# Kernel optimization log

Measured on AMD Instinct MI355X. Metric: run time of the kernel, lower is better.

The kernel has to match this reference:

```python
import jax, jax.numpy as jnp
import numpy as np

N_EXPERTS = 8
TOP_K = 2
AUX_COEF = 0.01
Z_COEF = 0.001


def setup_inputs() -> dict:
    key = jax.random.key(0)
    ks = jax.random.split(key, 5)
    B, S, D, F, E = 2, 2048, 768, 2048, N_EXPERTS
    std = 0.02
    std_out = std / np.sqrt(2 * 12)  # scale_init_by_depth, n_layers=12
    return {
        "x": jax.random.normal(ks[0], (B, S, D), jnp.float32),
        "router_w": jax.random.normal(ks[1], (D, E), jnp.float32) * std,
        "w1": jax.random.normal(ks[2], (E, D, F), jnp.float32) * std,
        "w2": jax.random.normal(ks[3], (E, F, D), jnp.float32) * std_out,
        "w3": jax.random.normal(ks[4], (E, D, F), jnp.float32) * std,
    }


def reference(x, router_w, w1, w2, w3):
    B, S, D = x.shape
    E = w1.shape[0]
    x_flat = x.reshape(-1, D)                      # [N, D]
    n_tokens = x_flat.shape[0]

    router_logits = x_flat @ router_w               # [N, E]
    probs = jax.nn.softmax(router_logits.astype(jnp.float32), axis=-1)
    topk_w, topk_i = jax.lax.top_k(probs, TOP_K)    # [N, K]
    topk_w = topk_w / jnp.sum(topk_w, axis=-1, keepdims=True)

    # Combine: equivalent to sort/group dispatch + per-expert GEMM + index_add,
    # expressed as a masked per-expert (fixed, small E) dense pass.
    out = jnp.zeros((n_tokens, D), dtype=x.dtype)
    for e in range(E):
        gate = jnp.sum(jnp.where(topk_i == e, topk_w, 0.0), axis=-1)  # [N] f32
        h = jax.nn.silu(x_flat @ w1[e]) * (x_flat @ w3[e])            # [N, F]
        out = out + gate[:, None].astype(x.dtype) * (h @ w2[e])

    # Switch-style load-balancing aux loss + z-loss
    importance = probs.mean(axis=0)                 # [E]
    top1 = topk_i[:, 0]
    load = jnp.zeros((E,), jnp.float32).at[top1].add(1.0) / n_tokens
    aux_loss = E * jnp.sum(importance * load) * AUX_COEF
    z_loss = jnp.mean(router_logits.astype(jnp.float32) ** 2) * Z_COEF

    return out.reshape(B, S, D), aux_loss, z_loss
```

## Files before the change

### kernel.cpp

```cpp
#include <hip/hip_runtime.h>
#include <hip/hip_bf16.h>

constexpr int NT = 4096;
constexpr int DD = 768;
constexpr int FF = 2048;
constexpr int NE = 8;
constexpr int MAXROWS = 9216;
constexpr int MAXMT128 = 72;
constexpr int MAXMT256 = 40;
constexpr int NKT1 = DD / 64;
constexpr int NKT2 = FF / 64;

constexpr int IDX_CNTA   = 0;
constexpr int IDX_CNTT1  = 8;
constexpr int IDX_CUR    = 16;
constexpr int IDX_IMP    = 24;
constexpr int IDX_ZSUM   = 32;
constexpr int IDX_NTILES = 33;
constexpr int IDX_OFF    = 34;
constexpr int IDX_EXPT   = 48;
constexpr int IDX_N256   = 120;
constexpr int IDX_E256   = 128;
constexpr int IDX_B256   = 168;
constexpr int IDX_L256   = 208;

constexpr size_t OFF_META   = 0;
constexpr size_t OFF_TKE    = 1024;
constexpr size_t OFF_GATE   = OFF_TKE    + (size_t)NT*2*4;
constexpr size_t OFF_ROWOF  = OFF_GATE   + (size_t)NT*2*4;
constexpr size_t OFF_TOKROW = OFF_ROWOF  + (size_t)NT*2*4;
constexpr size_t OFF_XG     = 136192;
constexpr size_t OFF_W1T    = OFF_XG  + (size_t)MAXROWS*DD*2;
constexpr size_t OFF_W3T    = OFF_W1T + (size_t)NE*FF*DD*2;
constexpr size_t OFF_W2T    = OFF_W3T + (size_t)NE*FF*DD*2;
constexpr size_t OFF_H      = OFF_W2T + (size_t)NE*FF*DD*2;
constexpr size_t OFF_OP     = OFF_H   + (size_t)MAXROWS*FF*2;

typedef float f32x4 __attribute__((ext_vector_type(4)));
typedef __bf16 bf16x8v __attribute__((ext_vector_type(8)));
typedef unsigned short u16x8 __attribute__((ext_vector_type(8)));

__device__ inline unsigned short f2bf_bits(float f) {
  __bf16 h = (__bf16)f;
  return *(unsigned short*)&h;
}
__device__ inline float bf2f(unsigned short u) {
  unsigned v = (unsigned)u << 16;
  return *(float*)&v;
}

__device__ __forceinline__ void glds16(const void* g, void* l) {
  __builtin_amdgcn_global_load_lds(
      (const __attribute__((address_space(1))) unsigned int*)g,
      (__attribute__((address_space(3))) unsigned int*)l, 16, 0, 0);
}

constexpr int RB = 128;
__global__ __launch_bounds__(256) void router_kernel(const float* __restrict__ x,
    const float* __restrict__ rw, int* __restrict__ meta,
    int* __restrict__ tke, float* __restrict__ gateArr) {
  __shared__ float s_imp[NE];
  __shared__ float s_z;
  __shared__ int s_cnt1[NE], s_cnta[NE];
  if (threadIdx.x < NE) { s_imp[threadIdx.x] = 0.f; s_cnt1[threadIdx.x] = 0; s_cnta[threadIdx.x] = 0; }
  if (threadIdx.x == 0) s_z = 0.f;
  __syncthreads();

  const int wave = threadIdx.x >> 6, lane = threadIdx.x & 63;
  float impacc[NE];
  #pragma unroll
  for (int e = 0; e < NE; ++e) impacc[e] = 0.f;
  float zacc = 0.f;

  for (int t = blockIdx.x * 4 + wave; t < NT; t += RB * 4) {
    float acc[NE];
    #pragma unroll
    for (int e = 0; e < NE; ++e) acc[e] = 0.f;
    const float* xr = x + (size_t)t * DD;
    for (int i = lane; i < DD; i += 64) {
      float xv = xr[i];
      const float* r = rw + i * NE;
      #pragma unroll
      for (int e = 0; e < NE; ++e) acc[e] += xv * r[e];
    }
    #pragma unroll
    for (int off = 32; off > 0; off >>= 1) {
      #pragma unroll
      for (int e = 0; e < NE; ++e) acc[e] += __shfl_xor(acc[e], off);
    }
    float mx = acc[0];
    #pragma unroll
    for (int e = 1; e < NE; ++e) mx = fmaxf(mx, acc[e]);
    float p[NE]; float s = 0.f;
    #pragma unroll
    for (int e = 0; e < NE; ++e) { p[e] = __expf(acc[e] - mx); s += p[e]; }
    float inv = 1.f / s;
    #pragma unroll
    for (int e = 0; e < NE; ++e) p[e] *= inv;
    int e0 = 0; float p0 = p[0];
    #pragma unroll
    for (int e = 1; e < NE; ++e) if (p[e] > p0) { p0 = p[e]; e0 = e; }
    int e1 = -1; float p1 = -1.f;
    #pragma unroll
    for (int e = 0; e < NE; ++e) if (e != e0 && p[e] > p1) { p1 = p[e]; e1 = e; }
    if (lane == 0) {
      #pragma unroll
      for (int e = 0; e < NE; ++e) { impacc[e] += p[e]; zacc += acc[e] * acc[e]; }
      atomicAdd(&s_cnt1[e0], 1);
      atomicAdd(&s_cnta[e0], 1);
      atomicAdd(&s_cnta[e1], 1);
      float gs = 1.f / (p0 + p1);
      tke[t*2]   = e0; tke[t*2+1] = e1;
      gateArr[t*2] = p0 * gs; gateArr[t*2+1] = p1 * gs;
    }
  }
  if (lane == 0) {
    #pragma unroll
    for (int e = 0; e < NE; ++e) atomicAdd(&s_imp[e], impacc[e]);
    atomicAdd(&s_z, zacc);
  }
  __syncthreads();
  float* fmeta = (float*)meta;
  if (threadIdx.x < NE) {
    atomicAdd(&fmeta[IDX_IMP + threadIdx.x], s_imp[threadIdx.x]);
    atomicAdd(&meta[IDX_CNTT1 + threadIdx.x], s_cnt1[threadIdx.x]);
    atomicAdd(&meta[IDX_CNTA + threadIdx.x], s_cnta[threadIdx.x]);
  }
  if (threadIdx.x == NE) atomicAdd(&fmeta[IDX_ZSUM], s_z);
}

__global__ __launch_bounds__(128) void scan_kernel(int* __restrict__ meta,
                                                   float* __restrict__ out_tail) {
  __shared__ int s_off[NE + 1];
  __shared__ int s_nt[NE];
  __shared__ float s_aux;
  const int t = threadIdx.x;
  if (t < NE) s_nt[t] = (meta[IDX_CNTA + t] + 127) >> 7;
  __syncthreads();
  if (t == 0) {
    int off = 0;
    for (int e = 0; e < NE; ++e) { s_off[e] = off; off += s_nt[e]; }
    s_off[NE] = off;
  }
  __syncthreads();
  const int ntiles = s_off[NE];
  if (t < NE) meta[IDX_OFF + t] = s_off[t] << 7;
  if (t == NE) { meta[IDX_OFF + NE] = ntiles << 7; meta[IDX_NTILES] = ntiles; }
  if (t < ntiles) {
    int e = 0;
    while (t >= s_off[e + 1]) e++;
    meta[IDX_EXPT + t] = e;
  }
  if (t == 0) {
    int n2t = 0;
    for (int e = 0; e < NE; ++e) {
      const int base = s_off[e] << 7;
      const int lim  = base + (s_nt[e] << 7);
      const int n2 = (s_nt[e] + 1) >> 1;
      for (int i = 0; i < n2; ++i) {
        meta[IDX_E256 + n2t] = e;
        meta[IDX_B256 + n2t] = base + (i << 8);
        meta[IDX_L256 + n2t] = lim;
        ++n2t;
      }
    }
    meta[IDX_N256] = n2t;
  }
  float* fmeta = (float*)meta;
  float pl = 0.f;
  if (t < NE)
    pl = (fmeta[IDX_IMP + t] / (float)NT) * ((float)meta[IDX_CNTT1 + t] / (float)NT);
  if (t < 64) {
    #pragma unroll
    for (int off = 4; off > 0; off >>= 1) pl += __shfl_xor(pl, off);
    if (t == 0) s_aux = pl;
  }
  __syncthreads();
  if (t == 0) {
    out_tail[0] = (float)NE * s_aux * 0.01f;
    out_tail[1] = fmeta[IDX_ZSUM] / (float)(NT * NE) * 0.001f;
  }
}

__global__ __launch_bounds__(256) void scatter_kernel(const int* __restrict__ tke,
    int* __restrict__ meta, int* __restrict__ rowof, int* __restrict__ tokrow) {
  __shared__ int s_cnt[NE], s_base[NE];
  const int t = blockIdx.x * 256 + threadIdx.x;
  if (threadIdx.x < NE) s_cnt[threadIdx.x] = 0;
  __syncthreads();
  const int e0 = tke[t*2], e1 = tke[t*2 + 1];
  const int l0 = atomicAdd(&s_cnt[e0], 1);
  const int l1 = atomicAdd(&s_cnt[e1], 1);
  __syncthreads();
  if (threadIdx.x < NE)
    s_base[threadIdx.x] = atomicAdd(&meta[IDX_CUR + threadIdx.x], s_cnt[threadIdx.x]);
  __syncthreads();
  const int r0 = meta[IDX_OFF + e0] + s_base[e0] + l0;
  const int r1 = meta[IDX_OFF + e1] + s_base[e1] + l1;
  rowof[t*2]     = r0;
  rowof[t*2 + 1] = r1;
  tokrow[r0] = t;
  tokrow[r1] = t;
}

__global__ __launch_bounds__(192) void gather_kernel(const float* __restrict__ x,
    const int* __restrict__ tokrow, const int* __restrict__ meta,
    __bf16* __restrict__ Xg) {
  const int row = blockIdx.x;
  if (row >= meta[IDX_OFF + NE]) return;
  const int tok = tokrow[row];
  ushort4* dst = (ushort4*)(Xg + (size_t)row * DD);
  const int i = threadIdx.x;
  ushort4 o;
  if (tok >= 0) {
    float4 v = ((const float4*)(x + (size_t)tok * DD))[i];
    o.x = f2bf_bits(v.x); o.y = f2bf_bits(v.y);
    o.z = f2bf_bits(v.z); o.w = f2bf_bits(v.w);
  } else {
    o.x = o.y = o.z = o.w = 0;
  }
  dst[i] = o;
}

constexpr int TS = 68;
__global__ __launch_bounds__(256) void transpose_cvt_all(
    const float* __restrict__ w1, const float* __restrict__ w3,
    const float* __restrict__ w2, __bf16* __restrict__ W1t,
    __bf16* __restrict__ W3t, __bf16* __restrict__ W2t) {
  const int z = blockIdx.z, which = z >> 3, e = z & 7;
  const float* src; __bf16* dst; int R, C, rt, ct;
  if (which == 0)      { src = w1; dst = W1t; R = DD; C = FF; rt = blockIdx.y; ct = blockIdx.x; }
  else if (which == 1) { src = w3; dst = W3t; R = DD; C = FF; rt = blockIdx.y; ct = blockIdx.x; }
  else                 { src = w2; dst = W2t; R = FF; C = DD; rt = blockIdx.x; ct = blockIdx.y; }
  src += (size_t)e * DD * FF; dst += (size_t)e * DD * FF;
  const int r0 = rt * 64, c0 = ct * 64;
  __shared__ __align__(16) __bf16 tile[64 * TS];
  const int t = threadIdx.x;
  #pragma unroll
  for (int i = 0; i < 4; ++i) {
    int idx = t + i * 256; int r = idx >> 4, q = idx & 15;
    float4 v = *(const float4*)&src[(size_t)(r0 + r) * C + c0 + q * 4];
    ushort4 o;
    o.x = f2bf_bits(v.x); o.y = f2bf_bits(v.y);
    o.z = f2bf_bits(v.z); o.w = f2bf_bits(v.w);
    *(ushort4*)&tile[r * TS + q * 4] = o;
  }
  __syncthreads();
  #pragma unroll
  for (int i = 0; i < 2; ++i) {
    int idx = t + i * 256; int c = idx >> 3, seg = idx & 7;
    u16x8 o;
    #pragma unroll
    for (int k = 0; k < 8; ++k)
      o[k] = *(unsigned short*)&tile[(seg * 8 + k) * TS + c];
    *(u16x8*)&dst[(size_t)(c0 + c) * R + r0 + seg * 8] = o;
  }
}

__global__ __launch_bounds__(512, 2) void gemm1_kernel(
    const __bf16* __restrict__ Xg, const __bf16* __restrict__ W1t,
    const __bf16* __restrict__ W3t, __bf16* __restrict__ Hb,
    const int* __restrict__ meta) {
  const int mt = blockIdx.y;
  if (mt >= meta[IDX_N256]) return;
  const int e      = meta[IDX_E256 + mt];
  const int m0     = meta[IDX_B256 + mt];
  const int rowlim = meta[IDX_L256 + mt];
  const int n0 = blockIdx.x * 128;

  __shared__ __align__(16) __bf16 As[2][256 * 64];
  __shared__ __align__(16) __bf16 Bs[2][256 * 64];

  const int t = threadIdx.x, lane = t & 63, wid = t >> 6;
  const int wm = wid >> 2, wn = wid & 3;
  const int lane15 = lane & 15, g = lane >> 4;

  const __bf16* __restrict__ W1e = W1t + (size_t)e * FF * DD;
  const __bf16* __restrict__ W3e = W3t + (size_t)e * FF * DD;

  const int aBase = (wm * 128 + lane15) * 64;
  const int bBase = (wn * 64 + lane15) * 64;
  const int c0 = ((g    ) ^ (lane & 7)) * 8;
  const int c1 = ((4 + g) ^ (lane & 7)) * 8;

  const int o0v = t, o1v = 512 + t;
  const int r0v = o0v >> 3, r1v = o1v >> 3;
  const int cl0 = (o0v & 7) ^ (r0v & 7), cl1 = (o1v & 7) ^ (r1v & 7);
  int gA00 = m0 + r0v;        if (gA00 >= MAXROWS) gA00 = 0;
  int gA01 = m0 + r1v;        if (gA01 >= MAXROWS) gA01 = 0;
  int gA10 = m0 + 128 + r0v;  if (gA10 >= MAXROWS) gA10 = 0;
  int gA11 = m0 + 128 + r1v;  if (gA11 >= MAXROWS) gA11 = 0;
  const __bf16* aS00 = Xg + (size_t)gA00 * DD + cl0 * 8;
  const __bf16* aS01 = Xg + (size_t)gA01 * DD + cl1 * 8;
  const __bf16* aS10 = Xg + (size_t)gA10 * DD + cl0 * 8;
  const __bf16* aS11 = Xg + (size_t)gA11 * DD + cl1 * 8;
  const int fc0 = n0 + ((r0v >> 5) << 4) + (r0v & 15);
  const int fc1 = n0 + ((r1v >> 5) << 4) + (r1v & 15);
  const __bf16* bW0 = (r0v & 16) ? W3e : W1e;
  const __bf16* bW1 = (r1v & 16) ? W3e : W1e;
  const __bf16* bS00 = bW0 + (size_t)fc0 * DD + cl0 * 8;
  const __bf16* bS01 = bW1 + (size_t)fc1 * DD + cl1 * 8;
  const __bf16* bS10 = bW0 + (size_t)(fc0 + 64) * DD + cl0 * 8;
  const __bf16* bS11 = bW1 + (size_t)(fc1 + 64) * DD + cl1 * 8;
  const int L00 = (       wid * 64) * 8;
  const int L01 = ( 512 + wid * 64) * 8;
  const int L10 = (1024 + wid * 64) * 8;
  const int L11 = (1536 + wid * 64) * 8;

  auto st2 = [&](__bf16* dstBuf, int kt, const __bf16* s0, const __bf16* s1,
                 int d0, int d1) {
    glds16(s0 + (size_t)kt * 64, dstBuf + d0);
    glds16(s1 + (size_t)kt * 64, dstBuf + d1);
  };

  const f32x4 zero = {0.f, 0.f, 0.f, 0.f};
  f32x4 acc[8][4];
  #pragma unroll
  for (int i = 0; i < 8; ++i)
    #pragma unroll
    for (int j = 0; j < 4; ++j) acc[i][j] = zero;

  __bf16 *Ac = &As[0][0], *An = &As[1][0];
  __bf16 *Bc = &Bs[0][0], *Bn = &Bs[1][0];

  st2(Ac, 0, aS00, aS01, L00, L01); st2(Ac, 0, aS10, aS11, L10, L11);
  st2(Bc, 0, bS00, bS01, L00, L01); st2(Bc, 0, bS10, bS11, L10, L11);
  st2(An, 1, aS00, aS01, L00, L01); st2(An, 1, aS10, aS11, L10, L11);
  st2(Bn, 1, bS00, bS01, L00, L01); st2(Bn, 1, bS10, bS11, L10, L11);
  asm volatile("s_waitcnt vmcnt(8)" ::: "memory");
  __builtin_amdgcn_s_barrier();

  bf16x8v af[8], ag[8], bf[8];

  for (int k = 0; k < NKT1; ++k) {
    const bool k2ok = (k < NKT1 - 2);
    #pragma unroll
    for (int i = 0; i < 4; ++i) {
      af[i*2+0] = *(const bf16x8v*)&Ac[aBase + i*1024 + c0];
      af[i*2+1] = *(const bf16x8v*)&Ac[aBase + i*1024 + c1];
    }
    #pragma unroll
    for (int j = 0; j < 4; ++j) {
      bf[j*2+0] = *(const bf16x8v*)&Bc[bBase + j*1024 + c0];
      bf[j*2+1] = *(const bf16x8v*)&Bc[bBase + j*1024 + c1];
    }
    __builtin_amdgcn_s_barrier();
    asm volatile("s_waitcnt lgkmcnt(0)" ::: "memory");
    __builtin_amdgcn_s_setprio(1);
    #pragma unroll
    for (int i = 0; i < 4; ++i)
      #pragma unroll
      for (int j = 0; j < 2; ++j) {
        acc[i][j] = __builtin_amdgcn_mfma_f32_16x16x32_bf16(af[i*2+0], bf[j*2+0], acc[i][j], 0, 0, 0);
        acc[i][j] = __builtin_amdgcn_mfma_f32_16x16x32_bf16(af[i*2+1], bf[j*2+1], acc[i][j], 0, 0, 0);
      }
    __builtin_amdgcn_s_setprio(0);
    __builtin_amdgcn_s_barrier();

    #pragma unroll
    for (int i = 0; i < 4; ++i) {
      ag[i*2+0] = *(const bf16x8v*)&Ac[aBase + (4+i)*1024 + c0];
      ag[i*2+1] = *(const bf16x8v*)&Ac[aBase + (4+i)*1024 + c1];
    }
    if (k2ok) st2(Bc, k + 2, bS00, bS01, L00, L01);
    __builtin_amdgcn_s_barrier();
    asm volatile("s_waitcnt lgkmcnt(0)" ::: "memory");
    __builtin_amdgcn_s_setprio(1);
    #pragma unroll
    for (int i = 0; i < 4; ++i)
      #pragma unroll
      for (int j = 0; j < 2; ++j) {
        acc[4+i][j] = __builtin_amdgcn_mfma_f32_16x16x32_bf16(ag[i*2+0], bf[j*2+0], acc[4+i][j], 0, 0, 0);
        acc[4+i][j] = __builtin_amdgcn_mfma_f32_16x16x32_bf16(ag[i*2+1], bf[j*2+1], acc[4+i][j], 0, 0, 0);
      }
    __builtin_amdgcn_s_setprio(0);
    __builtin_amdgcn_s_barrier();

    if (k2ok) {
      st2(Ac, k + 2, aS00, aS01, L00, L01);
      st2(Bc, k + 2, bS10, bS11, L10, L11);
    }
    __builtin_amdgcn_s_barrier();
    __builtin_amdgcn_s_setprio(1);
    #pragma unroll
    for (int i = 0; i < 4; ++i)
      #pragma unroll
      for (int j = 0; j < 2; ++j) {
        acc[i][2+j] = __builtin_amdgcn_mfma_f32_16x16x32_bf16(af[i*2+0], bf[(2+j)*2+0], acc[i][2+j], 0, 0, 0);
        acc[i][2+j] = __builtin_amdgcn_mfma_f32_16x16x32_bf16(af[i*2+1], bf[(2+j)*2+1], acc[i][2+j], 0, 0, 0);
      }
    __builtin_amdgcn_s_setprio(0);
    __builtin_amdgcn_s_barrier();

    if (k2ok) st2(Ac, k + 2, aS10, aS11, L10, L11);
    __builtin_amdgcn_s_barrier();
    __builtin_amdgcn_s_setprio(1);
    #pragma unroll
    for (int i = 0; i < 4; ++i)
      #pragma unroll
      for (int j = 0; j < 2; ++j) {
        acc[4+i][2+j] = __builtin_amdgcn_mfma_f32_16x16x32_bf16(ag[i*2+0], bf[(2+j)*2+0], acc[4+i][2+j], 0, 0, 0);
        acc[4+i][2+j] = __builtin_amdgcn_mfma_f32_16x16x32_bf16(ag[i*2+1], bf[(2+j)*2+1], acc[4+i][2+j], 0, 0, 0);
      }
    __builtin_amdgcn_s_setprio(0);
    if (k2ok)               { asm volatile("s_waitcnt vmcnt(8)" ::: "memory"); }
    else if (k == NKT1 - 2) { asm volatile("s_waitcnt vmcnt(0)" ::: "memory"); }
    __builtin_amdgcn_s_barrier();

    __bf16* tp;
    tp = Ac; Ac = An; An = tp;
    tp = Bc; Bc = Bn; Bn = tp;
  }

  #pragma unroll
  for (int i = 0; i < 8; ++i) {
    const int grow = m0 + wm * 128 + i * 16 + (lane >> 4) * 4;
    #pragma unroll
    for (int p = 0; p < 2; ++p) {
      const int col = n0 + (wn * 2 + p) * 16 + lane15;
      const f32x4 v1 = acc[i][2*p], v3 = acc[i][2*p + 1];
      #pragma unroll
      for (int r = 0; r < 4; ++r) {
        if (grow + r < rowlim) {
          float h = v1[r] / (1.f + __expf(-v1[r])) * v3[r];
          Hb[(size_t)(grow + r) * FF + col] = (__bf16)h;
        }
      }
    }
  }
}

__global__ __launch_bounds__(512, 2) void gemm2_kernel(
    const __bf16* __restrict__ Hb, const __bf16* __restrict__ W2t,
    __bf16* __restrict__ OP, const int* __restrict__ meta) {
  const int mt = blockIdx.y;
  if (mt >= meta[IDX_N256]) return;
  const int e      = meta[IDX_E256 + mt];
  const int m0     = meta[IDX_B256 + mt];
  const int rowlim = meta[IDX_L256 + mt];
  const int n0 = blockIdx.x * 128;

  __shared__ __align__(16) __bf16 As[2][256 * 64];
  __shared__ __align__(16) __bf16 Bs[2][128 * 64];

  const int t = threadIdx.x, lane = t & 63, wid = t >> 6;
  const int wm = wid >> 2, wn = wid & 3;
  const int lane15 = lane & 15, g = lane >> 4;

  const __bf16* __restrict__ W2e = W2t + (size_t)e * DD * FF;

  const int aBase = (wm * 128 + lane15) * 64;
  const int bBase = (wn * 32 + lane15) * 64;
  const int c0 = ((g    ) ^ (lane & 7)) * 8;
  const int c1 = ((4 + g) ^ (lane & 7)) * 8;

  const int o0v = t, o1v = 512 + t;
  const int r0v = o0v >> 3, r1v = o1v >> 3;
  const int cl0 = (o0v & 7) ^ (r0v & 7), cl1 = (o1v & 7) ^ (r1v & 7);
  const int L00 = (       wid * 64) * 8;
  const int L01 = ( 512 + wid * 64) * 8;
  const int L10 = (1024 + wid * 64) * 8;
  const int L11 = (1536 + wid * 64) * 8;

  int gA00 = m0 + r0v;        if (gA00 >= MAXROWS) gA00 = 0;
  int gA01 = m0 + r1v;        if (gA01 >= MAXROWS) gA01 = 0;
  int gA10 = m0 + 128 + r0v;  if (gA10 >= MAXROWS) gA10 = 0;
  int gA11 = m0 + 128 + r1v;  if (gA11 >= MAXROWS) gA11 = 0;
  const __bf16* aS00 = Hb + (size_t)gA00 * FF + cl0 * 8;
  const __bf16* aS01 = Hb + (size_t)gA01 * FF + cl1 * 8;
  const __bf16* aS10 = Hb + (size_t)gA10 * FF + cl0 * 8;
  const __bf16* aS11 = Hb + (size_t)gA11 * FF + cl1 * 8;
  const __bf16* bS0  = W2e + (size_t)(n0 + r0v) * FF + cl0 * 8;
  const __bf16* bS1  = W2e + (size_t)(n0 + r1v) * FF + cl1 * 8;

  auto stA = [&](__bf16* d, int kt) {
    glds16(aS00 + (size_t)kt * 64, d + L00);
    glds16(aS01 + (size_t)kt * 64, d + L01);
    glds16(aS10 + (size_t)kt * 64, d + L10);
    glds16(aS11 + (size_t)kt * 64, d + L11);
  };
  auto stB = [&](__bf16* d, int kt) {
    glds16(bS0 + (size_t)kt * 64, d + L00);
    glds16(bS1 + (size_t)kt * 64, d + L01);
  };

  const f32x4 zero = {0.f, 0.f, 0.f, 0.f};
  f32x4 acc[8][2];
  #pragma unroll
  for (int i = 0; i < 8; ++i)
    #pragma unroll
    for (int j = 0; j < 2; ++j) acc[i][j] = zero;

  __bf16 *Ac = &As[0][0], *An = &As[1][0];
  __bf16 *Bc = &Bs[0][0], *Bn = &Bs[1][0];

  stA(Ac, 0); stB(Bc, 0);
  stA(An, 1); stB(Bn, 1);
  asm volatile("s_waitcnt vmcnt(6)" ::: "memory");
  __builtin_amdgcn_s_barrier();

  bf16x8v af[8], ag[8], bfr[4];

  for (int k = 0; k < NKT2; ++k) {
    const bool k2ok = (k < NKT2 - 2);
    #pragma unroll
    for (int i = 0; i < 4; ++i) {
      af[i*2+0] = *(const bf16x8v*)&Ac[aBase + i*1024 + c0];
      af[i*2+1] = *(const bf16x8v*)&Ac[aBase + i*1024 + c1];
    }
    #pragma unroll
    for (int i = 0; i < 4; ++i) {
      ag[i*2+0] = *(const bf16x8v*)&Ac[aBase + (4+i)*1024 + c0];
      ag[i*2+1] = *(const bf16x8v*)&Ac[aBase + (4+i)*1024 + c1];
    }
    #pragma unroll
    for (int j = 0; j < 2; ++j) {
      bfr[j*2+0] = *(const bf16x8v*)&Bc[bBase + j*1024 + c0];
      bfr[j*2+1] = *(const bf16x8v*)&Bc[bBase + j*1024 + c1];
    }
    __builtin_amdgcn_s_barrier();
    asm volatile("s_waitcnt lgkmcnt(0)" ::: "memory");
    __builtin_amdgcn_s_setprio(1);
    #pragma unroll
    for (int i = 0; i < 4; ++i)
      #pragma unroll
      for (int j = 0; j < 2; ++j) {
        acc[i][j] = __builtin_amdgcn_mfma_f32_16x16x32_bf16(af[i*2+0], bfr[j*2+0], acc[i][j], 0, 0, 0);
        acc[i][j] = __builtin_amdgcn_mfma_f32_16x16x32_bf16(af[i*2+1], bfr[j*2+1], acc[i][j], 0, 0, 0);
      }
    __builtin_amdgcn_s_setprio(0);
    __builtin_amdgcn_s_barrier();

    if (k2ok) { stA(Ac, k + 2); stB(Bc, k + 2); }
    __builtin_amdgcn_s_setprio(1);
    #pragma unroll
    for (int i = 0; i < 4; ++i)
      #pragma unroll
      for (int j = 0; j < 2; ++j) {
        acc[4+i][j] = __builtin_amdgcn_mfma_f32_16x16x32_bf16(ag[i*2+0], bfr[j*2+0], acc[4+i][j], 0, 0, 0);
        acc[4+i][j] = __builtin_amdgcn_mfma_f32_16x16x32_bf16(ag[i*2+1], bfr[j*2+1], acc[4+i][j], 0, 0, 0);
      }
    __builtin_amdgcn_s_setprio(0);
    if (k2ok)               { asm volatile("s_waitcnt vmcnt(6)" ::: "memory"); }
    else if (k == NKT2 - 2) { asm volatile("s_waitcnt vmcnt(0)" ::: "memory"); }
    __builtin_amdgcn_s_barrier();

    __bf16* tp;
    tp = Ac; Ac = An; An = tp;
    tp = Bc; Bc = Bn; Bn = tp;
  }

  #pragma unroll
  for (int i = 0; i < 8; ++i) {
    const int rowb = m0 + wm * 128 + i * 16 + (lane >> 4) * 4;
    #pragma unroll
    for (int jj = 0; jj < 2; ++jj) {
      const int col = n0 + wn * 32 + jj * 16 + lane15;
      #pragma unroll
      for (int r = 0; r < 4; ++r)
        if (rowb + r < rowlim)
          OP[(size_t)(rowb + r) * DD + col] = (__bf16)acc[i][jj][r];
    }
  }
}

__global__ __launch_bounds__(192) void combine_kernel(const __bf16* __restrict__ OP,
    const int* __restrict__ rowof, const float* __restrict__ gateArr,
    float* __restrict__ out) {
  const int t = blockIdx.x;
  const int r0 = rowof[t*2], r1 = rowof[t*2 + 1];
  const float g0 = gateArr[t*2], g1 = gateArr[t*2 + 1];
  const ushort4* p0 = (const ushort4*)(OP + (size_t)r0 * DD);
  const ushort4* p1 = (const ushort4*)(OP + (size_t)r1 * DD);
  const int i = threadIdx.x;
  ushort4 a = p0[i], b = p1[i];
  float4 o;
  o.x = g0 * bf2f(a.x) + g1 * bf2f(b.x);
  o.y = g0 * bf2f(a.y) + g1 * bf2f(b.y);
  o.z = g0 * bf2f(a.z) + g1 * bf2f(b.z);
  o.w = g0 * bf2f(a.w) + g1 * bf2f(b.w);
  ((float4*)(out + (size_t)t * DD))[i] = o;
}

extern "C" void kernel_launch(void* const* d_in, const int* in_sizes, int n_in,
                              void* d_out, int out_size, void* d_ws, size_t ws_size,
                              hipStream_t stream) {
  const float* x  = (const float*)d_in[0];
  const float* rw = (const float*)d_in[1];
  const float* w1 = (const float*)d_in[2];
  const float* w2 = (const float*)d_in[3];
  const float* w3 = (const float*)d_in[4];
  float* out = (float*)d_out;

  char* ws = (char*)d_ws;
  int*    meta   = (int*)(ws + OFF_META);
  int*    tke    = (int*)(ws + OFF_TKE);
  float*  gateA  = (float*)(ws + OFF_GATE);
  int*    rowof  = (int*)(ws + OFF_ROWOF);
  int*    tokrow = (int*)(ws + OFF_TOKROW);
  __bf16* Xg     = (__bf16*)(ws + OFF_XG);
  __bf16* W1t    = (__bf16*)(ws + OFF_W1T);
  __bf16* W3t    = (__bf16*)(ws + OFF_W3T);
  __bf16* W2t    = (__bf16*)(ws + OFF_W2T);
  __bf16* Hb     = (__bf16*)(ws + OFF_H);
  __bf16* OP     = (__bf16*)(ws + OFF_OP);

  hipMemsetAsync(ws + OFF_META, 0, 1024, stream);
  hipMemsetAsync(ws + OFF_TOKROW, 0xFF, (size_t)MAXROWS * 4, stream);

  transpose_cvt_all<<<dim3(32, 12, 24), 256, 0, stream>>>(w1, w3, w2, W1t, W3t, W2t);

  router_kernel<<<RB, 256, 0, stream>>>(x, rw, meta, tke, gateA);
  scan_kernel<<<1, 128, 0, stream>>>(meta, out + (size_t)NT * DD);
  scatter_kernel<<<NT/256, 256, 0, stream>>>(tke, meta, rowof, tokrow);
  gather_kernel<<<MAXROWS, 192, 0, stream>>>(x, tokrow, meta, Xg);

  gemm1_kernel<<<dim3(FF/128, MAXMT256), 512, 0, stream>>>(Xg, W1t, W3t, Hb, meta);
  gemm2_kernel<<<dim3(DD/128, MAXMT256), 512, 0, stream>>>(Hb, W2t, OP, meta);
  combine_kernel<<<NT, 192, 0, stream>>>(OP, rowof, gateA, out);
}
```

Baseline: 391.3 us.

## Fuse weight transpose with router and fold combine into gemm2 via atomics

Merges the weight transpose/convert kernel and the router kernel into one launch, with block-index ranges selecting the role, so the router can overlap the transpose. Drops the combine kernel and the bf16 OP buffer: gemm2 now scales each output row by a per-row gate and atomically adds it in fp32 into the zeroed output, using tokrow to find the token. This removes a launch and a round-trip of the intermediate, but adds a memset of the output and scattered float atomics in gemm2's epilogue. Because the summation order of the two expert contributions is no longer fixed, results may vary slightly between runs.

```diff
diff --git a/kernel.cpp b/kernel.cpp
--- a/kernel.cpp
+++ b/kernel.cpp
@@ -34,7 +34,7 @@
 constexpr size_t OFF_W3T    = OFF_W1T + (size_t)NE*FF*DD*2;
 constexpr size_t OFF_W2T    = OFF_W3T + (size_t)NE*FF*DD*2;
 constexpr size_t OFF_H      = OFF_W2T + (size_t)NE*FF*DD*2;
-constexpr size_t OFF_OP     = OFF_H   + (size_t)MAXROWS*FF*2;
+constexpr size_t OFF_RGATE  = OFF_H   + (size_t)MAXROWS*FF*2;
 
 typedef float f32x4 __attribute__((ext_vector_type(4)));
 typedef __bf16 bf16x8v __attribute__((ext_vector_type(8)));
@@ -43,10 +43,6 @@
 __device__ inline unsigned short f2bf_bits(float f) {
   __bf16 h = (__bf16)f;
   return *(unsigned short*)&h;
-}
-__device__ inline float bf2f(unsigned short u) {
-  unsigned v = (unsigned)u << 16;
-  return *(float*)&v;
 }
 
 __device__ __forceinline__ void glds16(const void* g, void* l) {
@@ -56,77 +52,118 @@
 }
 
 constexpr int RB = 128;
-__global__ __launch_bounds__(256) void router_kernel(const float* __restrict__ x,
-    const float* __restrict__ rw, int* __restrict__ meta,
-    int* __restrict__ tke, float* __restrict__ gateArr) {
-  __shared__ float s_imp[NE];
-  __shared__ float s_z;
-  __shared__ int s_cnt1[NE], s_cnta[NE];
-  if (threadIdx.x < NE) { s_imp[threadIdx.x] = 0.f; s_cnt1[threadIdx.x] = 0; s_cnta[threadIdx.x] = 0; }
-  if (threadIdx.x == 0) s_z = 0.f;
-  __syncthreads();
-
-  const int wave = threadIdx.x >> 6, lane = threadIdx.x & 63;
-  float impacc[NE];
-  #pragma unroll
-  for (int e = 0; e < NE; ++e) impacc[e] = 0.f;
-  float zacc = 0.f;
-
-  for (int t = blockIdx.x * 4 + wave; t < NT; t += RB * 4) {
-    float acc[NE];
-    #pragma unroll
-    for (int e = 0; e < NE; ++e) acc[e] = 0.f;
-    const float* xr = x + (size_t)t * DD;
-    for (int i = lane; i < DD; i += 64) {
-      float xv = xr[i];
-      const float* r = rw + i * NE;
-      #pragma unroll
-      for (int e = 0; e < NE; ++e) acc[e] += xv * r[e];
-    }
-    #pragma unroll
-    for (int off = 32; off > 0; off >>= 1) {
-      #pragma unroll
-      for (int e = 0; e < NE; ++e) acc[e] += __shfl_xor(acc[e], off);
-    }
-    float mx = acc[0];
-    #pragma unroll
-    for (int e = 1; e < NE; ++e) mx = fmaxf(mx, acc[e]);
-    float p[NE]; float s = 0.f;
-    #pragma unroll
-    for (int e = 0; e < NE; ++e) { p[e] = __expf(acc[e] - mx); s += p[e]; }
-    float inv = 1.f / s;
-    #pragma unroll
-    for (int e = 0; e < NE; ++e) p[e] *= inv;
-    int e0 = 0; float p0 = p[0];
-    #pragma unroll
-    for (int e = 1; e < NE; ++e) if (p[e] > p0) { p0 = p[e]; e0 = e; }
-    int e1 = -1; float p1 = -1.f;
-    #pragma unroll
-    for (int e = 0; e < NE; ++e) if (e != e0 && p[e] > p1) { p1 = p[e]; e1 = e; }
+constexpr int TS = 68;
+__global__ __launch_bounds__(256) void prep_kernel(
+    const float* __restrict__ w1, const float* __restrict__ w3,
+    const float* __restrict__ w2, __bf16* __restrict__ W1t,
+    __bf16* __restrict__ W3t, __bf16* __restrict__ W2t,
+    const float* __restrict__ x, const float* __restrict__ rw,
+    int* __restrict__ meta, int* __restrict__ tke,
+    float* __restrict__ gateArr) {
+  const int bid = blockIdx.x;
+  if (bid < 9216) {
+    const int bz = bid / 384;
+    const int rem = bid - bz * 384;
+    const int by = rem >> 5, bx = rem & 31;
+    const int which = bz >> 3, e = bz & 7;
+    const float* src; __bf16* dst; int R, C, rt, ct;
+    if (which == 0)      { src = w1; dst = W1t; R = DD; C = FF; rt = by; ct = bx; }
+    else if (which == 1) { src = w3; dst = W3t; R = DD; C = FF; rt = by; ct = bx; }
+    else                 { src = w2; dst = W2t; R = FF; C = DD; rt = bx; ct = by; }
+    src += (size_t)e * DD * FF; dst += (size_t)e * DD * FF;
+    const int r0 = rt * 64, c0 = ct * 64;
+    __shared__ __align__(16) __bf16 tile[64 * TS];
+    const int t = threadIdx.x;
+    #pragma unroll
+    for (int i = 0; i < 4; ++i) {
+      int idx = t + i * 256; int r = idx >> 4, q = idx & 15;
+      float4 v = *(const float4*)&src[(size_t)(r0 + r) * C + c0 + q * 4];
+      ushort4 o;
+      o.x = f2bf_bits(v.x); o.y = f2bf_bits(v.y);
+      o.z = f2bf_bits(v.z); o.w = f2bf_bits(v.w);
+      *(ushort4*)&tile[r * TS + q * 4] = o;
+    }
+    __syncthreads();
+    #pragma unroll
+    for (int i = 0; i < 2; ++i) {
+      int idx = t + i * 256; int c = idx >> 3, seg = idx & 7;
+      u16x8 o;
+      #pragma unroll
+      for (int k = 0; k < 8; ++k)
+        o[k] = *(unsigned short*)&tile[(seg * 8 + k) * TS + c];
+      *(u16x8*)&dst[(size_t)(c0 + c) * R + r0 + seg * 8] = o;
+    }
+  } else {
+    const int rb = bid - 9216;
+    __shared__ float s_imp[NE];
+    __shared__ float s_z;
+    __shared__ int s_cnt1[NE], s_cnta[NE];
+    if (threadIdx.x < NE) { s_imp[threadIdx.x] = 0.f; s_cnt1[threadIdx.x] = 0; s_cnta[threadIdx.x] = 0; }
+    if (threadIdx.x == 0) s_z = 0.f;
+    __syncthreads();
+
+    const int wave = threadIdx.x >> 6, lane = threadIdx.x & 63;
+    float impacc[NE];
+    #pragma unroll
+    for (int e = 0; e < NE; ++e) impacc[e] = 0.f;
+    float zacc = 0.f;
+
+    for (int t = rb * 4 + wave; t < NT; t += RB * 4) {
+      float acc[NE];
+      #pragma unroll
+      for (int e = 0; e < NE; ++e) acc[e] = 0.f;
+      const float* xr = x + (size_t)t * DD;
+      for (int i = lane; i < DD; i += 64) {
+        float xv = xr[i];
+        const float* r = rw + i * NE;
+        #pragma unroll
+        for (int e = 0; e < NE; ++e) acc[e] += xv * r[e];
+      }
+      #pragma unroll
+      for (int off = 32; off > 0; off >>= 1) {
+        #pragma unroll
+        for (int e = 0; e < NE; ++e) acc[e] += __shfl_xor(acc[e], off);
+      }
+      float mx = acc[0];
+      #pragma unroll
+      for (int e = 1; e < NE; ++e) mx = fmaxf(mx, acc[e]);
+      float p[NE]; float s = 0.f;
+      #pragma unroll
+      for (int e = 0; e < NE; ++e) { p[e] = __expf(acc[e] - mx); s += p[e]; }
+      float inv = 1.f / s;
+      #pragma unroll
+      for (int e = 0; e < NE; ++e) p[e] *= inv;
+      int e0 = 0; float p0 = p[0];
+      #pragma unroll
+      for (int e = 1; e < NE; ++e) if (p[e] > p0) { p0 = p[e]; e0 = e; }
+      int e1 = -1; float p1 = -1.f;
+      #pragma unroll
+      for (int e = 0; e < NE; ++e) if (e != e0 && p[e] > p1) { p1 = p[e]; e1 = e; }
+      if (lane == 0) {
+        #pragma unroll
+        for (int e = 0; e < NE; ++e) { impacc[e] += p[e]; zacc += acc[e] * acc[e]; }
+        atomicAdd(&s_cnt1[e0], 1);
+        atomicAdd(&s_cnta[e0], 1);
+        atomicAdd(&s_cnta[e1], 1);
+        float gs = 1.f / (p0 + p1);
+        tke[t*2]   = e0; tke[t*2+1] = e1;
+        gateArr[t*2] = p0 * gs; gateArr[t*2+1] = p1 * gs;
+      }
+    }
     if (lane == 0) {
       #pragma unroll
-      for (int e = 0; e < NE; ++e) { impacc[e] += p[e]; zacc += acc[e] * acc[e]; }
-      atomicAdd(&s_cnt1[e0], 1);
-      atomicAdd(&s_cnta[e0], 1);
-      atomicAdd(&s_cnta[e1], 1);
-      float gs = 1.f / (p0 + p1);
-      tke[t*2]   = e0; tke[t*2+1] = e1;
-      gateArr[t*2] = p0 * gs; gateArr[t*2+1] = p1 * gs;
-    }
-  }
-  if (lane == 0) {
-    #pragma unroll
-    for (int e = 0; e < NE; ++e) atomicAdd(&s_imp[e], impacc[e]);
-    atomicAdd(&s_z, zacc);
-  }
-  __syncthreads();
-  float* fmeta = (float*)meta;
-  if (threadIdx.x < NE) {
-    atomicAdd(&fmeta[IDX_IMP + threadIdx.x], s_imp[threadIdx.x]);
-    atomicAdd(&meta[IDX_CNTT1 + threadIdx.x], s_cnt1[threadIdx.x]);
-    atomicAdd(&meta[IDX_CNTA + threadIdx.x], s_cnta[threadIdx.x]);
-  }
-  if (threadIdx.x == NE) atomicAdd(&fmeta[IDX_ZSUM], s_z);
+      for (int e = 0; e < NE; ++e) atomicAdd(&s_imp[e], impacc[e]);
+      atomicAdd(&s_z, zacc);
+    }
+    __syncthreads();
+    float* fmeta = (float*)meta;
+    if (threadIdx.x < NE) {
+      atomicAdd(&fmeta[IDX_IMP + threadIdx.x], s_imp[threadIdx.x]);
+      atomicAdd(&meta[IDX_CNTT1 + threadIdx.x], s_cnt1[threadIdx.x]);
+      atomicAdd(&meta[IDX_CNTA + threadIdx.x], s_cnta[threadIdx.x]);
+    }
+    if (threadIdx.x == NE) atomicAdd(&fmeta[IDX_ZSUM], s_z);
+  }
 }
 
 __global__ __launch_bounds__(128) void scan_kernel(int* __restrict__ meta,
@@ -183,7 +220,8 @@
 }
 
 __global__ __launch_bounds__(256) void scatter_kernel(const int* __restrict__ tke,
-    int* __restrict__ meta, int* __restrict__ rowof, int* __restrict__ tokrow) {
+    int* __restrict__ meta, int* __restrict__ tokrow,
+    float* __restrict__ rowgate, const float* __restrict__ gateArr) {
   __shared__ int s_cnt[NE], s_base[NE];
   const int t = blockIdx.x * 256 + threadIdx.x;
   if (threadIdx.x < NE) s_cnt[threadIdx.x] = 0;
@@ -197,10 +235,10 @@
   __syncthreads();
   const int r0 = meta[IDX_OFF + e0] + s_base[e0] + l0;
   const int r1 = meta[IDX_OFF + e1] + s_base[e1] + l1;
-  rowof[t*2]     = r0;
-  rowof[t*2 + 1] = r1;
   tokrow[r0] = t;
   tokrow[r1] = t;
+  rowgate[r0] = gateArr[t*2];
+  rowgate[r1] = gateArr[t*2 + 1];
 }
 
 __global__ __launch_bounds__(192) void gather_kernel(const float* __restrict__ x,
@@ -220,41 +258,6 @@
     o.x = o.y = o.z = o.w = 0;
   }
   dst[i] = o;
-}
-
-constexpr int TS = 68;
-__global__ __launch_bounds__(256) void transpose_cvt_all(
-    const float* __restrict__ w1, const float* __restrict__ w3,
-    const float* __restrict__ w2, __bf16* __restrict__ W1t,
-    __bf16* __restrict__ W3t, __bf16* __restrict__ W2t) {
-  const int z = blockIdx.z, which = z >> 3, e = z & 7;
-  const float* src; __bf16* dst; int R, C, rt, ct;
-  if (which == 0)      { src = w1; dst = W1t; R = DD; C = FF; rt = blockIdx.y; ct = blockIdx.x; }
-  else if (which == 1) { src = w3; dst = W3t; R = DD; C = FF; rt = blockIdx.y; ct = blockIdx.x; }
-  else                 { src = w2; dst = W2t; R = FF; C = DD; rt = blockIdx.x; ct = blockIdx.y; }
-  src += (size_t)e * DD * FF; dst += (size_t)e * DD * FF;
-  const int r0 = rt * 64, c0 = ct * 64;
-  __shared__ __align__(16) __bf16 tile[64 * TS];
-  const int t = threadIdx.x;
-  #pragma unroll
-  for (int i = 0; i < 4; ++i) {
-    int idx = t + i * 256; int r = idx >> 4, q = idx & 15;
-    float4 v = *(const float4*)&src[(size_t)(r0 + r) * C + c0 + q * 4];
-    ushort4 o;
-    o.x = f2bf_bits(v.x); o.y = f2bf_bits(v.y);
-    o.z = f2bf_bits(v.z); o.w = f2bf_bits(v.w);
-    *(ushort4*)&tile[r * TS + q * 4] = o;
-  }
-  __syncthreads();
-  #pragma unroll
-  for (int i = 0; i < 2; ++i) {
-    int idx = t + i * 256; int c = idx >> 3, seg = idx & 7;
-    u16x8 o;
-    #pragma unroll
-    for (int k = 0; k < 8; ++k)
-      o[k] = *(unsigned short*)&tile[(seg * 8 + k) * TS + c];
-    *(u16x8*)&dst[(size_t)(c0 + c) * R + r0 + seg * 8] = o;
-  }
 }
 
 __global__ __launch_bounds__(512, 2) void gemm1_kernel(
@@ -432,7 +435,8 @@
 
 __global__ __launch_bounds__(512, 2) void gemm2_kernel(
     const __bf16* __restrict__ Hb, const __bf16* __restrict__ W2t,
-    __bf16* __restrict__ OP, const int* __restrict__ meta) {
+    float* __restrict__ outp, const int* __restrict__ meta,
+    const int* __restrict__ tokrow, const float* __restrict__ rowgate) {
   const int mt = blockIdx.y;
   if (mt >= meta[IDX_N256]) return;
   const int e      = meta[IDX_E256 + mt];
@@ -554,32 +558,21 @@
   for (int i = 0; i < 8; ++i) {
     const int rowb = m0 + wm * 128 + i * 16 + (lane >> 4) * 4;
     #pragma unroll
-    for (int jj = 0; jj < 2; ++jj) {
-      const int col = n0 + wn * 32 + jj * 16 + lane15;
-      #pragma unroll
-      for (int r = 0; r < 4; ++r)
-        if (rowb + r < rowlim)
-          OP[(size_t)(rowb + r) * DD + col] = (__bf16)acc[i][jj][r];
-    }
-  }
-}
-
-__global__ __launch_bounds__(192) void combine_kernel(const __bf16* __restrict__ OP,
-    const int* __restrict__ rowof, const float* __restrict__ gateArr,
-    float* __restrict__ out) {
-  const int t = blockIdx.x;
-  const int r0 = rowof[t*2], r1 = rowof[t*2 + 1];
-  const float g0 = gateArr[t*2], g1 = gateArr[t*2 + 1];
-  const ushort4* p0 = (const ushort4*)(OP + (size_t)r0 * DD);
-  const ushort4* p1 = (const ushort4*)(OP + (size_t)r1 * DD);
-  const int i = threadIdx.x;
-  ushort4 a = p0[i], b = p1[i];
-  float4 o;
-  o.x = g0 * bf2f(a.x) + g1 * bf2f(b.x);
-  o.y = g0 * bf2f(a.y) + g1 * bf2f(b.y);
-  o.z = g0 * bf2f(a.z) + g1 * bf2f(b.z);
-  o.w = g0 * bf2f(a.w) + g1 * bf2f(b.w);
-  ((float4*)(out + (size_t)t * DD))[i] = o;
+    for (int r = 0; r < 4; ++r) {
+      const int row = rowb + r;
+      if (row < rowlim) {
+        const int tok = tokrow[row];
+        if (tok >= 0) {
+          const float gv = rowgate[row];
+          #pragma unroll
+          for (int jj = 0; jj < 2; ++jj) {
+            const int col = n0 + wn * 32 + jj * 16 + lane15;
+            atomicAdd(&outp[(size_t)tok * DD + col], gv * acc[i][jj][r]);
+          }
+        }
+      }
+    }
+  }
 }
 
 extern "C" void kernel_launch(void* const* d_in, const int* in_sizes, int n_in,
@@ -596,26 +589,25 @@
   int*    meta   = (int*)(ws + OFF_META);
   int*    tke    = (int*)(ws + OFF_TKE);
   float*  gateA  = (float*)(ws + OFF_GATE);
-  int*    rowof  = (int*)(ws + OFF_ROWOF);
   int*    tokrow = (int*)(ws + OFF_TOKROW);
   __bf16* Xg     = (__bf16*)(ws + OFF_XG);
   __bf16* W1t    = (__bf16*)(ws + OFF_W1T);
   __bf16* W3t    = (__bf16*)(ws + OFF_W3T);
   __bf16* W2t    = (__bf16*)(ws + OFF_W2T);
   __bf16* Hb     = (__bf16*)(ws + OFF_H);
-  __bf16* OP     = (__bf16*)(ws + OFF_OP);
+  float*  rgate  = (float*)(ws + OFF_RGATE);
 
   hipMemsetAsync(ws + OFF_META, 0, 1024, stream);
   hipMemsetAsync(ws + OFF_TOKROW, 0xFF, (size_t)MAXROWS * 4, stream);
-
-  transpose_cvt_all<<<dim3(32, 12, 24), 256, 0, stream>>>(w1, w3, w2, W1t, W3t, W2t);
-
-  router_kernel<<<RB, 256, 0, stream>>>(x, rw, meta, tke, gateA);
+  hipMemsetAsync(out, 0, (size_t)NT * DD * 4, stream);
+
+  prep_kernel<<<9344, 256, 0, stream>>>(w1, w3, w2, W1t, W3t, W2t,
+                                        x, rw, meta, tke, gateA);
   scan_kernel<<<1, 128, 0, stream>>>(meta, out + (size_t)NT * DD);
-  scatter_kernel<<<NT/256, 256, 0, stream>>>(tke, meta, rowof, tokrow);
+  scatter_kernel<<<NT/256, 256, 0, stream>>>(tke, meta, tokrow, rgate, gateA);
   gather_kernel<<<MAXROWS, 192, 0, stream>>>(x, tokrow, meta, Xg);
 
   gemm1_kernel<<<dim3(FF/128, MAXMT256), 512, 0, stream>>>(Xg, W1t, W3t, Hb, meta);
-  gemm2_kernel<<<dim3(DD/128, MAXMT256), 512, 0, stream>>>(Hb, W2t, OP, meta);
-  combine_kernel<<<NT, 192, 0, stream>>>(OP, rowof, gateA, out);
-}
+  gemm2_kernel<<<dim3(DD/128, MAXMT256), 512, 0, stream>>>(Hb, W2t, out, meta,
+                                                           tokrow, rgate);
+}
```

After: 413.4 us. +5.6%, slower.
